# Kernel tuning notes

Hardware: AMD Instinct MI355X
Metric: run time of the kernel (lower is better)

Reference implementation:

```python
import jax, jax.numpy as jnp
import numpy as np

N, E, DIN, DH, ED, H, C = 50000, 800000, 384, 256, 32, 4, 64
EPS = 1e-5


def setup_inputs() -> dict:
    key = jax.random.key(0)
    ks = jax.random.split(key, 32)
    w = lambda k, shape, fan: (jax.random.normal(k, shape, jnp.float32) / np.float32(np.sqrt(fan)))
    inp = {
        'x': jax.random.normal(ks[0], (N, DIN), jnp.float32),
        'edge_index': jax.random.randint(ks[1], (2, E), 0, N, dtype=jnp.int32),
        'edge_attr': jax.random.normal(ks[2], (E, ED), jnp.float32),
        'W_in': w(ks[3], (DIN, DH), DIN), 'b_in': jnp.zeros((DH,), jnp.float32),
        'W_out': w(ks[4], (DH, DH), DH), 'b_out': jnp.zeros((DH,), jnp.float32),
    }
    for i in range(2):
        o = 5 + 6 * i
        inp[f'Wl{i}'] = w(ks[o + 0], (DH, H * C), DH)
        inp[f'bl{i}'] = jnp.zeros((H * C,), jnp.float32)
        inp[f'Wr{i}'] = w(ks[o + 1], (DH, H * C), DH)
        inp[f'br{i}'] = jnp.zeros((H * C,), jnp.float32)
        inp[f'We{i}'] = w(ks[o + 2], (ED, H * C), ED)
        inp[f'att{i}'] = w(ks[o + 3], (H, C), C)
        inp[f'bias{i}'] = jnp.zeros((H * C,), jnp.float32)
        inp[f'g{i}'] = jnp.ones((DH,), jnp.float32)
        inp[f'beta{i}'] = jnp.zeros((DH,), jnp.float32)
    return inp


def _gatv2(h, src, dst, ea, Wl, bl, Wr, br, We, att, bias):
    # h: [N, DH]; src/dst: [Etot]; ea: [Etot, ED]
    xl = (h @ Wl + bl).reshape(N, H, C)
    xr = (h @ Wr + br).reshape(N, H, C)
    ee = (ea @ We).reshape(-1, H, C)
    m = jax.nn.leaky_relu(xl[src] + xr[dst] + ee, 0.2)  # [Etot,H,C]
    logits = jnp.einsum('ehc,hc->eh', m, att)           # [Etot,H]
    mx = jax.ops.segment_max(logits, dst, num_segments=N)
    p = jnp.exp(logits - mx[dst])
    den = jax.ops.segment_sum(p, dst, num_segments=N)
    alpha = p / den[dst]                                # softmax per dst node
    out = jax.ops.segment_sum(xl[src] * alpha[:, :, None], dst, num_segments=N)
    return out.reshape(N, H * C) + bias


def _graph_norm(h, g, beta):
    # PyG LayerNorm(mode='graph'), batch=None: normalize over all nodes & channels
    mu = h.mean()
    hc = h - mu
    var = (hc * hc).mean()
    return hc / jnp.sqrt(var + EPS) * g + beta


def reference(x, edge_index, edge_attr, W_in, b_in,
              Wl0, bl0, Wr0, br0, We0, att0, bias0, g0, beta0,
              Wl1, bl1, Wr1, br1, We1, att1, bias1, g1, beta1,
              W_out, b_out):
    loops = jnp.arange(N, dtype=edge_index.dtype)
    src = jnp.concatenate([edge_index[0], loops])
    dst = jnp.concatenate([edge_index[1], loops])
    # self-loop edge_attr filled with mean edge feature (PyG fill_value='mean')
    ea = jnp.concatenate([edge_attr, jnp.broadcast_to(edge_attr.mean(0), (N, ED))], axis=0)
    h = jax.nn.relu(x @ W_in + b_in)
    layers = ((Wl0, bl0, Wr0, br0, We0, att0, bias0, g0, beta0),
              (Wl1, bl1, Wr1, br1, We1, att1, bias1, g1, beta1))
    for Wl, bl, Wr, br, We, att, bias, g, beta in layers:
        hn = jax.nn.elu(_gatv2(h, src, dst, ea, Wl, bl, Wr, br, We, att, bias))
        h = _graph_norm(h + hn, g, beta)
    return h @ W_out + b_out
```

## Files before the change

### kernel.cpp

```cpp
#include <hip/hip_runtime.h>
#include <hip/hip_bf16.h>

#define N_NODES 50000
#define E_EDGES 800000
#define DIN_K   384
#define DH_N    256
#define EPSN    1e-5f

typedef unsigned short ushortT;
typedef __attribute__((ext_vector_type(4))) float f32x4;
typedef __attribute__((ext_vector_type(8))) short bf16x8;

static __device__ __forceinline__ float bf2f(unsigned short u)
{
    return __uint_as_float(((unsigned)u) << 16);
}
static __device__ __forceinline__ unsigned short f2bf(float f)
{
    unsigned u = __float_as_uint(f);
    unsigned r = (u + 0x7fffu + ((u >> 16) & 1u)) >> 16;
    return (unsigned short)r;
}
static __device__ __forceinline__ unsigned pack2(float a, float b)
{
    return (unsigned)f2bf(a) | ((unsigned)f2bf(b) << 16);
}

__global__ __launch_bounds__(256) void ea_accum_kernel(const float* __restrict__ ea,
                                                       float* __restrict__ accum, long total)
{
    long stride = (long)gridDim.x * blockDim.x;
    float local = 0.f;
    for (long i = (long)blockIdx.x * blockDim.x + threadIdx.x; i < total; i += stride)
        local += ea[i];
    __shared__ float red[256];
    red[threadIdx.x] = local;
    __syncthreads();
    if (threadIdx.x < 32) {
        float s = 0.f;
#pragma unroll
        for (int r = 0; r < 8; ++r) s += red[r * 32 + threadIdx.x];
        atomicAdd(&accum[threadIdx.x], s);
    }
}

__global__ void hist_kernel(const int* __restrict__ dst, int* __restrict__ counts, int E)
{
    int stride = gridDim.x * blockDim.x;
    for (int e = blockIdx.x * blockDim.x + threadIdx.x; e < E; e += stride)
        atomicAdd(&counts[dst[e]], 1);
}

__global__ __launch_bounds__(1024) void scan_kernel(const int* __restrict__ counts,
                                                    int* __restrict__ offsets, int Nn)
{
    __shared__ int sdata[1024];
    __shared__ int run_s;
    int tid = threadIdx.x;
    if (tid == 0) run_s = 0;
    __syncthreads();
    for (int base2 = 0; base2 < Nn; base2 += 1024) {
        int i = base2 + tid;
        int v = (i < Nn) ? counts[i] : 0;
        sdata[tid] = v;
        __syncthreads();
        for (int off = 1; off < 1024; off <<= 1) {
            int t = (tid >= off) ? sdata[tid - off] : 0;
            __syncthreads();
            sdata[tid] += t;
            __syncthreads();
        }
        int run = run_s;
        if (i < Nn) offsets[i] = run + sdata[tid] - v;
        int tot = sdata[1023];
        __syncthreads();
        if (tid == 0) run_s = run + tot;
        __syncthreads();
    }
    if (tid == 0) offsets[Nn] = run_s;
}

__global__ void scatter_kernel(const int* __restrict__ src, const int* __restrict__ dst,
                               const int* __restrict__ offsets, int* __restrict__ cursors,
                               int* __restrict__ s_src, int* __restrict__ s_dst,
                               int* __restrict__ s_eid, int E)
{
    int stride = gridDim.x * blockDim.x;
    for (int e = blockIdx.x * blockDim.x + threadIdx.x; e < E; e += stride) {
        int d = dst[e];
        int p = offsets[d] + atomicAdd(&cursors[d], 1);
        s_src[p] = src[e];
        s_dst[p] = d;
        s_eid[p] = e;
    }
}

__global__ void eemean_kernel(const float* __restrict__ accum,
                              const float* __restrict__ We0, const float* __restrict__ We1,
                              float* __restrict__ eemean, float invE)
{
    int tid = threadIdx.x;
    int layer = tid >> 8, c = tid & 255;
    const float* W = layer ? We1 : We0;
    float s = 0.f;
#pragma unroll
    for (int j = 0; j < 32; ++j) s += accum[j] * invE * W[j * 256 + c];
    eemean[layer * 256 + c] = s;
}

__global__ __launch_bounds__(256) void transpose_bf16_kernel(const float* __restrict__ in,
                                                             ushortT* __restrict__ out,
                                                             int K, int N)
{
    __shared__ float tile[32][33];
    int bx = blockIdx.x * 32;
    int by = blockIdx.y * 32;
    int tx = threadIdx.x & 31, ty = threadIdx.x >> 5;
#pragma unroll
    for (int r = 0; r < 32; r += 8) {
        int k = by + ty + r, n = bx + tx;
        if (k < K && n < N) tile[ty + r][tx] = in[(size_t)k * N + n];
    }
    __syncthreads();
#pragma unroll
    for (int r = 0; r < 32; r += 8) {
        int n = bx + ty + r, k = by + tx;
        if (n < N && k < K) out[(size_t)n * K + k] = f2bf(tile[tx][ty + r]);
    }
}

__global__ void fuse_bias_kernel(const float* __restrict__ bl, const float* __restrict__ br,
                                 float* __restrict__ out)
{
    int i = threadIdx.x;
    out[i] = (i < 256) ? bl[i] : br[i - 256];
}

__global__ __launch_bounds__(256) void mfma_gemm_kernel(
    const float* __restrict__ A, const ushortT* __restrict__ Bt,
    const float* __restrict__ bias, float* __restrict__ Cf,
    ushortT* __restrict__ Cb, int K, int Nn, int act)
{
    __shared__ __align__(16) ushortT As[128 * 32];
    __shared__ __align__(16) ushortT Bs[128 * 32];
    int tid = threadIdx.x;
    int brow = blockIdx.x * 128;
    int bcol = blockIdx.y * 128;
    int lane = tid & 63, w = tid >> 6;
    int wr = w >> 1, wc = w & 1;
    int fr = lane & 15, fq = lane >> 4;

    f32x4 acc[4][4];
#pragma unroll
    for (int i = 0; i < 4; ++i)
#pragma unroll
        for (int j = 0; j < 4; ++j)
            acc[i][j] = (f32x4){0.f, 0.f, 0.f, 0.f};

    int r0 = tid >> 2, g0 = tid & 3;
    int r1 = r0 + 64;
    int arow0 = brow + r0, arow1 = brow + r1;
    bool av0 = arow0 < N_NODES, av1 = arow1 < N_NODES;
    const float* Ap0 = A + (size_t)arow0 * K + g0 * 8;
    const float* Ap1 = A + (size_t)arow1 * K + g0 * 8;
    const ushortT* Bp0 = Bt + (size_t)(bcol + r0) * K + g0 * 8;
    const ushortT* Bp1 = Bt + (size_t)(bcol + r1) * K + g0 * 8;
    uint4* asw0 = (uint4*)&As[(size_t)tid * 8];
    uint4* asw1 = (uint4*)&As[(size_t)(tid + 256) * 8];
    uint4* bsw0 = (uint4*)&Bs[(size_t)tid * 8];
    uint4* bsw1 = (uint4*)&Bs[(size_t)(tid + 256) * 8];

    for (int k0 = 0; k0 < K; k0 += 32) {
        float4 z = make_float4(0.f, 0.f, 0.f, 0.f);
        float4 fa0 = z, fa1 = z, fc0 = z, fc1 = z;
        if (av0) { fa0 = *(const float4*)(Ap0 + k0); fc0 = *(const float4*)(Ap0 + k0 + 4); }
        if (av1) { fa1 = *(const float4*)(Ap1 + k0); fc1 = *(const float4*)(Ap1 + k0 + 4); }
        uint4 ub0 = *(const uint4*)(Bp0 + k0);
        uint4 ub1 = *(const uint4*)(Bp1 + k0);
        uint4 ua0, ua1;
        ua0.x = pack2(fa0.x, fa0.y); ua0.y = pack2(fa0.z, fa0.w);
        ua0.z = pack2(fc0.x, fc0.y); ua0.w = pack2(fc0.z, fc0.w);
        ua1.x = pack2(fa1.x, fa1.y); ua1.y = pack2(fa1.z, fa1.w);
        ua1.z = pack2(fc1.x, fc1.y); ua1.w = pack2(fc1.z, fc1.w);
        __syncthreads();
        *asw0 = ua0; *asw1 = ua1;
        *bsw0 = ub0; *bsw1 = ub1;
        __syncthreads();

        bf16x8 af[4], bfv[4];
#pragma unroll
        for (int mi = 0; mi < 4; ++mi)
            af[mi] = *(bf16x8*)&As[(size_t)(wr * 64 + mi * 16 + fr) * 32 + fq * 8];
#pragma unroll
        for (int ni = 0; ni < 4; ++ni)
            bfv[ni] = *(bf16x8*)&Bs[(size_t)(wc * 64 + ni * 16 + fr) * 32 + fq * 8];
#pragma unroll
        for (int mi = 0; mi < 4; ++mi)
#pragma unroll
            for (int ni = 0; ni < 4; ++ni)
                acc[mi][ni] = __builtin_amdgcn_mfma_f32_16x16x32_bf16(
                    af[mi], bfv[ni], acc[mi][ni], 0, 0, 0);
    }

#pragma unroll
    for (int ni = 0; ni < 4; ++ni) {
        int col = bcol + wc * 64 + ni * 16 + fr;
        float bv = bias[col];
#pragma unroll
        for (int mi = 0; mi < 4; ++mi) {
#pragma unroll
            for (int r = 0; r < 4; ++r) {
                int row = brow + wr * 64 + mi * 16 + fq * 4 + r;
                if (row < N_NODES) {
                    float t = acc[mi][ni][r] + bv;
                    if (act == 1) t = t > 0.f ? t : 0.f;
                    if (Cf) Cf[(size_t)row * Nn + col] = t;
                    if (Cb) Cb[(size_t)row * Nn + col] = f2bf(t);
                }
            }
        }
    }
}

__global__ __launch_bounds__(256) void edge_logits_kernel(
    const float* __restrict__ ea, const int* __restrict__ s_eid,
    const int* __restrict__ s_src, const int* __restrict__ s_dst,
    const ushortT* __restrict__ Wet, const float* __restrict__ att,
    const ushortT* __restrict__ xlr, float* __restrict__ logits)
{
    __shared__ __align__(16) ushortT Wet_lds[256 * 40];
    __shared__ float att_lds[256];
    __shared__ int sidx[64], didx[64], eidv[64];
    int tid = threadIdx.x;
    int brow = blockIdx.x * 64;

#pragma unroll
    for (int t = 0; t < 4; ++t) {
        int f = tid + t * 256;
        int row = f >> 2, q = f & 3;
        *(uint4*)&Wet_lds[row * 40 + q * 8] = *(const uint4*)(Wet + (size_t)row * 32 + q * 8);
    }
    att_lds[tid] = att[tid];
    if (tid < 64) {
        sidx[tid] = s_src[brow + tid];
        didx[tid] = s_dst[brow + tid];
        eidv[tid] = s_eid[brow + tid];
    }
    __syncthreads();

    int lane = tid & 63, w = tid >> 6;
    int fr = lane & 15, fq = lane >> 4;
    int e_lane = w * 16 + fr;

    int eid = eidv[e_lane];
    const float* earow = ea + (size_t)eid * 32 + fq * 8;
    float4 f0 = ((const float4*)earow)[0];
    float4 f1 = ((const float4*)earow)[1];
    union { unsigned u[4]; bf16x8 v; } ub;
    ub.u[0] = pack2(f0.x, f0.y);
    ub.u[1] = pack2(f0.z, f0.w);
    ub.u[2] = pack2(f1.x, f1.y);
    ub.u[3] = pack2(f1.z, f1.w);
    bf16x8 bfrag = ub.v;

    f32x4 acc[16];
#pragma unroll
    for (int mi = 0; mi < 16; ++mi) {
        bf16x8 afrag = *(bf16x8*)&Wet_lds[(mi * 16 + fr) * 40 + fq * 8];
        acc[mi] = __builtin_amdgcn_mfma_f32_16x16x32_bf16(
            afrag, bfrag, (f32x4){0.f, 0.f, 0.f, 0.f}, 0, 0, 0);
    }

    int sn = sidx[e_lane], dn = didx[e_lane];
    const ushortT* lxp = xlr + (size_t)sn * 512;
    const ushortT* rxp = xlr + (size_t)dn * 512 + 256;
    float part[4] = {0.f, 0.f, 0.f, 0.f};
#pragma unroll
    for (int mi = 0; mi < 16; ++mi) {
        int ch = mi * 16 + fq * 4;
        ushort4 lx = *(const ushort4*)(lxp + ch);
        ushort4 rx = *(const ushort4*)(rxp + ch);
        float4 at = *(const float4*)&att_lds[ch];
        float t0 = acc[mi][0] + bf2f(lx.x) + bf2f(rx.x); t0 = t0 > 0.f ? t0 : 0.2f * t0;
        float t1 = acc[mi][1] + bf2f(lx.y) + bf2f(rx.y); t1 = t1 > 0.f ? t1 : 0.2f * t1;
        float t2 = acc[mi][2] + bf2f(lx.z) + bf2f(rx.z); t2 = t2 > 0.f ? t2 : 0.2f * t2;
        float t3 = acc[mi][3] + bf2f(lx.w) + bf2f(rx.w); t3 = t3 > 0.f ? t3 : 0.2f * t3;
        part[mi >> 2] += t0 * at.x + t1 * at.y + t2 * at.z + t3 * at.w;
    }
#pragma unroll
    for (int hh = 0; hh < 4; ++hh) {
        part[hh] += __shfl_xor(part[hh], 16);
        part[hh] += __shfl_xor(part[hh], 32);
    }
    if (fq == 0) {
        float4 o = make_float4(part[0], part[1], part[2], part[3]);
        *(float4*)&logits[(size_t)(brow + e_lane) * 4] = o;
    }
}

__global__ __launch_bounds__(256) void edge_attn_kernel(
    const int* __restrict__ s_src, const int* __restrict__ offsets,
    const float* __restrict__ logits,
    const float* __restrict__ att, const float* __restrict__ bias,
    const float* __restrict__ eemean,
    const ushortT* __restrict__ xlr, float* __restrict__ h)
{
    int lane = threadIdx.x & 63;
    int d = blockIdx.x * 4 + (threadIdx.x >> 6);
    size_t xbase = (size_t)d * 512 + lane * 4;
    size_t hbase = (size_t)d * 256 + lane * 4;
    int head = lane >> 4;

    ushort4 xlu = *(const ushort4*)(xlr + xbase);
    ushort4 xru = *(const ushort4*)(xlr + xbase + 256);
    float xr0 = bf2f(xru.x), xr1 = bf2f(xru.y), xr2 = bf2f(xru.z), xr3 = bf2f(xru.w);
    float xs0 = bf2f(xlu.x), xs1 = bf2f(xlu.y), xs2 = bf2f(xlu.z), xs3 = bf2f(xlu.w);
    float4 eem = *(const float4*)(eemean + lane * 4);
    float4 at4 = *(const float4*)(att + lane * 4);

    float m = -1e30f, s = 0.f;
    float acc0 = 0.f, acc1 = 0.f, acc2 = 0.f, acc3 = 0.f;
    int beg = offsets[d], end = offsets[d + 1];

    int idx1 = 0;
    ushort4 x_cur = make_ushort4(0, 0, 0, 0);
    float lg_cur = 0.f;
    if (beg < end) {
        int idx0 = s_src[beg];
        x_cur = *(const ushort4*)(xlr + (size_t)idx0 * 512 + lane * 4);
        lg_cur = logits[(size_t)beg * 4 + head];
        if (beg + 1 < end) idx1 = s_src[beg + 1];
    }

    for (int pos = beg; pos < end; ++pos) {
        ushort4 xv = x_cur;
        float lg = lg_cur;
        int np = pos + 1;
        if (np < end) {
            x_cur = *(const ushort4*)(xlr + (size_t)idx1 * 512 + lane * 4);
            lg_cur = logits[(size_t)np * 4 + head];
        }
        if (pos + 2 < end) idx1 = s_src[pos + 2];

        float nm = fmaxf(m, lg);
        float sc = __expf(m - nm);
        float pr = __expf(lg - nm);
        float v0 = bf2f(xv.x), v1 = bf2f(xv.y), v2 = bf2f(xv.z), v3 = bf2f(xv.w);
        s = s * sc + pr;
        acc0 = acc0 * sc + pr * v0;
        acc1 = acc1 * sc + pr * v1;
        acc2 = acc2 * sc + pr * v2;
        acc3 = acc3 * sc + pr * v3;
        m = nm;
    }

    {
        float t0 = xs0 + xr0 + eem.x; t0 = t0 > 0.f ? t0 : 0.2f * t0;
        float t1 = xs1 + xr1 + eem.y; t1 = t1 > 0.f ? t1 : 0.2f * t1;
        float t2 = xs2 + xr2 + eem.z; t2 = t2 > 0.f ? t2 : 0.2f * t2;
        float t3 = xs3 + xr3 + eem.w; t3 = t3 > 0.f ? t3 : 0.2f * t3;
        float lg = t0 * at4.x + t1 * at4.y + t2 * at4.z + t3 * at4.w;
        lg += __shfl_xor(lg, 1);
        lg += __shfl_xor(lg, 2);
        lg += __shfl_xor(lg, 4);
        lg += __shfl_xor(lg, 8);
        float nm = fmaxf(m, lg);
        float sc = __expf(m - nm);
        float pr = __expf(lg - nm);
        s = s * sc + pr;
        acc0 = acc0 * sc + pr * xs0;
        acc1 = acc1 * sc + pr * xs1;
        acc2 = acc2 * sc + pr * xs2;
        acc3 = acc3 * sc + pr * xs3;
    }

    float inv = 1.f / s;
    float4 b4 = *(const float4*)(bias + lane * 4);
    float4 hv = *(const float4*)(h + hbase);
    float o0 = acc0 * inv + b4.x; o0 = o0 > 0.f ? o0 : __expf(o0) - 1.f;
    float o1 = acc1 * inv + b4.y; o1 = o1 > 0.f ? o1 : __expf(o1) - 1.f;
    float o2 = acc2 * inv + b4.z; o2 = o2 > 0.f ? o2 : __expf(o2) - 1.f;
    float o3 = acc3 * inv + b4.w; o3 = o3 > 0.f ? o3 : __expf(o3) - 1.f;
    *(float4*)(h + hbase) = make_float4(hv.x + o0, hv.y + o1, hv.z + o2, hv.w + o3);
}

__global__ __launch_bounds__(256) void stats_kernel(const float* __restrict__ h,
                                                    float* __restrict__ stats)
{
    int stride = gridDim.x * blockDim.x;
    int total = N_NODES * 64;
    float ls = 0.f, lq = 0.f;
    for (int i = blockIdx.x * blockDim.x + threadIdx.x; i < total; i += stride) {
        float4 v = ((const float4*)h)[i];
        ls += v.x + v.y + v.z + v.w;
        lq += v.x * v.x + v.y * v.y + v.z * v.z + v.w * v.w;
    }
#pragma unroll
    for (int o = 1; o < 64; o <<= 1) {
        ls += __shfl_xor(ls, o);
        lq += __shfl_xor(lq, o);
    }
    __shared__ float red[8];
    int lane = threadIdx.x & 63, w = threadIdx.x >> 6;
    if (lane == 0) { red[w * 2] = ls; red[w * 2 + 1] = lq; }
    __syncthreads();
    if (threadIdx.x == 0) {
        atomicAdd(&stats[0], red[0] + red[2] + red[4] + red[6]);
        atomicAdd(&stats[1], red[1] + red[3] + red[5] + red[7]);
    }
}

__global__ void norm_finalize_kernel(float* __restrict__ stats)
{
    float invM = 1.f / ((float)N_NODES * 256.f);
    float mu = stats[0] * invM;
    float var = stats[1] * invM - mu * mu;
    stats[2] = mu;
    stats[3] = rsqrtf(var + EPSN);
}

__global__ void normalize_kernel(float* __restrict__ h, const float* __restrict__ g,
                                 const float* __restrict__ beta, const float* __restrict__ stats)
{
    float mu = stats[2], sc = stats[3];
    int stride = gridDim.x * blockDim.x;
    int total = N_NODES * 64;
    for (int i = blockIdx.x * blockDim.x + threadIdx.x; i < total; i += stride) {
        float4 v = ((float4*)h)[i];
        int k = (i & 63) * 4;
        float4 gv = *(const float4*)&g[k];
        float4 bv = *(const float4*)&beta[k];
        v.x = (v.x - mu) * sc * gv.x + bv.x;
        v.y = (v.y - mu) * sc * gv.y + bv.y;
        v.z = (v.z - mu) * sc * gv.z + bv.z;
        v.w = (v.w - mu) * sc * gv.w + bv.w;
        ((float4*)h)[i] = v;
    }
}

extern "C" void kernel_launch(void* const* d_in, const int* in_sizes, int n_in,
                              void* d_out, int out_size, void* d_ws, size_t ws_size,
                              hipStream_t stream)
{
    (void)in_sizes; (void)n_in; (void)out_size; (void)ws_size;
    const float* x     = (const float*)d_in[0];
    const int*   eidx  = (const int*)d_in[1];
    const float* ea    = (const float*)d_in[2];
    const float* W_in  = (const float*)d_in[3];
    const float* b_in  = (const float*)d_in[4];
    const float* W_out = (const float*)d_in[5];
    const float* b_out = (const float*)d_in[6];
    const float* Wl[2]  = {(const float*)d_in[7],  (const float*)d_in[16]};
    const float* bl[2]  = {(const float*)d_in[8],  (const float*)d_in[17]};
    const float* Wr[2]  = {(const float*)d_in[9],  (const float*)d_in[18]};
    const float* br[2]  = {(const float*)d_in[10], (const float*)d_in[19]};
    const float* We[2]  = {(const float*)d_in[11], (const float*)d_in[20]};
    const float* att[2] = {(const float*)d_in[12], (const float*)d_in[21]};
    const float* bias[2]= {(const float*)d_in[13], (const float*)d_in[22]};
    const float* g[2]   = {(const float*)d_in[14], (const float*)d_in[23]};
    const float* beta[2]= {(const float*)d_in[15], (const float*)d_in[24]};

    char* p = (char*)d_ws;
    auto take = [&](size_t bytes) -> char* {
        char* r = p;
        p += (bytes + 255) & ~(size_t)255;
        return r;
    };
    int*   counts  = (int*)take((size_t)N_NODES * 4);
    int*   cursors = (int*)take((size_t)N_NODES * 4);
    float* ea_acc  = (float*)take(32 * 4);
    float* stats   = (float*)take(8 * 4);
    size_t zero_bytes = (size_t)(p - (char*)d_ws);
    int*   offsets = (int*)take((size_t)(N_NODES + 1) * 4);
    int*   s_src   = (int*)take((size_t)E_EDGES * 4);
    int*   s_dst   = (int*)take((size_t)E_EDGES * 4);
    int*   s_eid   = (int*)take((size_t)E_EDGES * 4);
    float* eemean  = (float*)take(512 * 4);
    ushortT* WtIn  = (ushortT*)take((size_t)256 * 384 * 2);
    ushortT* WtLR0 = (ushortT*)take((size_t)512 * 256 * 2);
    ushortT* WtLR1 = (ushortT*)take((size_t)512 * 256 * 2);
    ushortT* WtOut = (ushortT*)take((size_t)256 * 256 * 2);
    ushortT* Wet0  = (ushortT*)take((size_t)256 * 32 * 2);
    ushortT* Wet1  = (ushortT*)take((size_t)256 * 32 * 2);
    float* fb0     = (float*)take(512 * 4);
    float* fb1     = (float*)take(512 * 4);
    ushortT* xlr   = (ushortT*)take((size_t)N_NODES * 512 * 2);
    float* h       = (float*)take((size_t)N_NODES * 256 * 4);
    float* logits  = (float*)take((size_t)E_EDGES * 4 * 4);

    const ushortT* WtLR[2] = {WtLR0, WtLR1};
    const ushortT* Wet[2] = {Wet0, Wet1};
    const float* fb[2] = {fb0, fb1};

    const int* srcv = eidx;
    const int* dstv = eidx + E_EDGES;

    hipMemsetAsync(d_ws, 0, zero_bytes, stream);

    ea_accum_kernel<<<512, 256, 0, stream>>>(ea, ea_acc, (long)E_EDGES * 32);
    hist_kernel<<<1024, 256, 0, stream>>>(dstv, counts, E_EDGES);
    scan_kernel<<<1, 1024, 0, stream>>>(counts, offsets, N_NODES);
    scatter_kernel<<<1024, 256, 0, stream>>>(srcv, dstv, offsets, cursors,
                                             s_src, s_dst, s_eid, E_EDGES);
    eemean_kernel<<<1, 512, 0, stream>>>(ea_acc, We[0], We[1], eemean, 1.0f / (float)E_EDGES);

    transpose_bf16_kernel<<<dim3(8, 12), 256, 0, stream>>>(W_in, WtIn, 384, 256);
    transpose_bf16_kernel<<<dim3(8, 8), 256, 0, stream>>>(Wl[0], WtLR0, 256, 256);
    transpose_bf16_kernel<<<dim3(8, 8), 256, 0, stream>>>(Wr[0], WtLR0 + 256 * 256, 256, 256);
    transpose_bf16_kernel<<<dim3(8, 8), 256, 0, stream>>>(Wl[1], WtLR1, 256, 256);
    transpose_bf16_kernel<<<dim3(8, 8), 256, 0, stream>>>(Wr[1], WtLR1 + 256 * 256, 256, 256);
    transpose_bf16_kernel<<<dim3(8, 8), 256, 0, stream>>>(W_out, WtOut, 256, 256);
    transpose_bf16_kernel<<<dim3(8, 1), 256, 0, stream>>>(We[0], Wet0, 32, 256);
    transpose_bf16_kernel<<<dim3(8, 1), 256, 0, stream>>>(We[1], Wet1, 32, 256);
    fuse_bias_kernel<<<1, 512, 0, stream>>>(bl[0], br[0], fb0);
    fuse_bias_kernel<<<1, 512, 0, stream>>>(bl[1], br[1], fb1);

    mfma_gemm_kernel<<<dim3(391, 2), 256, 0, stream>>>(x, WtIn, b_in, h, nullptr, 384, 256, 1);

    for (int l = 0; l < 2; ++l) {
        mfma_gemm_kernel<<<dim3(391, 4), 256, 0, stream>>>(h, WtLR[l], fb[l], nullptr, xlr,
                                                           256, 512, 0);
        edge_logits_kernel<<<E_EDGES / 64, 256, 0, stream>>>(ea, s_eid, s_src, s_dst,
                                                             Wet[l], att[l], xlr, logits);
        edge_attn_kernel<<<N_NODES / 4, 256, 0, stream>>>(s_src, offsets, logits,
                                                          att[l], bias[l], eemean + l * 256,
                                                          xlr, h);
        stats_kernel<<<2048, 256, 0, stream>>>(h, stats + l * 4);
        norm_finalize_kernel<<<1, 1, 0, stream>>>(stats + l * 4);
        normalize_kernel<<<2048, 256, 0, stream>>>(h, g[l], beta[l], stats + l * 4);
    }
    mfma_gemm_kernel<<<dim3(391, 2), 256, 0, stream>>>(h, WtOut, b_out, (float*)d_out, nullptr,
                                                       256, 256, 0);
}
```

Baseline: 1.373 ms.

## Split edge attention into alpha and accumulate passes, fuse graph-norm stats

Reorders the edge-logit MFMA output rows so each lane owns one head's 64 contiguous channels, which allows 16-byte gathers and drops the cross-lane shuffle reduction. The online-softmax edge_attn kernel is split in two. A new alpha kernel computes per-destination softmax normalisers across 16 parallel edge slots and writes normalised alphas in place. An accum kernel then does a plain weighted gather-sum and also produces the graph-norm statistics, which removes the separate stats pass over h. The cost is an extra pass that reads and writes the logits array, plus a small self-alpha buffer.

```diff
diff --git a/kernel.cpp b/kernel.cpp
--- a/kernel.cpp
+++ b/kernel.cpp
@@ -24,6 +24,13 @@
 static __device__ __forceinline__ unsigned pack2(float a, float b)
 {
     return (unsigned)f2bf(a) | ((unsigned)f2bf(b) << 16);
+}
+static __device__ __forceinline__ void unpack8(uint4 u, float* f)
+{
+    f[0] = bf2f((ushortT)(u.x & 0xffff)); f[1] = bf2f((ushortT)(u.x >> 16));
+    f[2] = bf2f((ushortT)(u.y & 0xffff)); f[3] = bf2f((ushortT)(u.y >> 16));
+    f[4] = bf2f((ushortT)(u.z & 0xffff)); f[5] = bf2f((ushortT)(u.z >> 16));
+    f[6] = bf2f((ushortT)(u.w & 0xffff)); f[7] = bf2f((ushortT)(u.w >> 16));
 }
 
 __global__ __launch_bounds__(256) void ea_accum_kernel(const float* __restrict__ ea,
@@ -237,8 +244,10 @@
 #pragma unroll
     for (int t = 0; t < 4; ++t) {
         int f = tid + t * 256;
-        int row = f >> 2, q = f & 3;
-        *(uint4*)&Wet_lds[row * 40 + q * 8] = *(const uint4*)(Wet + (size_t)row * 32 + q * 8);
+        int sr = f >> 2, q = f & 3;
+        int mi = sr >> 4, j = sr & 15;
+        int ch = ((j >> 2) << 6) + mi * 4 + (j & 3);
+        *(uint4*)&Wet_lds[sr * 40 + q * 8] = *(const uint4*)(Wet + (size_t)ch * 32 + q * 8);
     }
     att_lds[tid] = att[tid];
     if (tid < 64) {
@@ -272,137 +281,155 @@
     }
 
     int sn = sidx[e_lane], dn = didx[e_lane];
-    const ushortT* lxp = xlr + (size_t)sn * 512;
-    const ushortT* rxp = xlr + (size_t)dn * 512 + 256;
-    float part[4] = {0.f, 0.f, 0.f, 0.f};
-#pragma unroll
-    for (int mi = 0; mi < 16; ++mi) {
-        int ch = mi * 16 + fq * 4;
-        ushort4 lx = *(const ushort4*)(lxp + ch);
-        ushort4 rx = *(const ushort4*)(rxp + ch);
-        float4 at = *(const float4*)&att_lds[ch];
-        float t0 = acc[mi][0] + bf2f(lx.x) + bf2f(rx.x); t0 = t0 > 0.f ? t0 : 0.2f * t0;
-        float t1 = acc[mi][1] + bf2f(lx.y) + bf2f(rx.y); t1 = t1 > 0.f ? t1 : 0.2f * t1;
-        float t2 = acc[mi][2] + bf2f(lx.z) + bf2f(rx.z); t2 = t2 > 0.f ? t2 : 0.2f * t2;
-        float t3 = acc[mi][3] + bf2f(lx.w) + bf2f(rx.w); t3 = t3 > 0.f ? t3 : 0.2f * t3;
-        part[mi >> 2] += t0 * at.x + t1 * at.y + t2 * at.z + t3 * at.w;
-    }
-#pragma unroll
-    for (int hh = 0; hh < 4; ++hh) {
-        part[hh] += __shfl_xor(part[hh], 16);
-        part[hh] += __shfl_xor(part[hh], 32);
-    }
-    if (fq == 0) {
-        float4 o = make_float4(part[0], part[1], part[2], part[3]);
-        *(float4*)&logits[(size_t)(brow + e_lane) * 4] = o;
-    }
-}
-
-__global__ __launch_bounds__(256) void edge_attn_kernel(
-    const int* __restrict__ s_src, const int* __restrict__ offsets,
-    const float* __restrict__ logits,
-    const float* __restrict__ att, const float* __restrict__ bias,
-    const float* __restrict__ eemean,
-    const ushortT* __restrict__ xlr, float* __restrict__ h)
+    const ushortT* lxp = xlr + (size_t)sn * 512 + fq * 64;
+    const ushortT* rxp = xlr + (size_t)dn * 512 + 256 + fq * 64;
+    const float* atp = &att_lds[fq * 64];
+    float lgsum = 0.f;
+#pragma unroll
+    for (int m2 = 0; m2 < 8; ++m2) {
+        uint4 lu = *(const uint4*)(lxp + m2 * 8);
+        uint4 ru = *(const uint4*)(rxp + m2 * 8);
+        float lf[8], rf[8];
+        unpack8(lu, lf);
+        unpack8(ru, rf);
+        float4 a0 = *(const float4*)(atp + m2 * 8);
+        float4 a1 = *(const float4*)(atp + m2 * 8 + 4);
+        f32x4 e0 = acc[2 * m2];
+        f32x4 e1 = acc[2 * m2 + 1];
+        float t0 = e0[0] + lf[0] + rf[0]; t0 = t0 > 0.f ? t0 : 0.2f * t0;
+        float t1 = e0[1] + lf[1] + rf[1]; t1 = t1 > 0.f ? t1 : 0.2f * t1;
+        float t2 = e0[2] + lf[2] + rf[2]; t2 = t2 > 0.f ? t2 : 0.2f * t2;
+        float t3 = e0[3] + lf[3] + rf[3]; t3 = t3 > 0.f ? t3 : 0.2f * t3;
+        float t4 = e1[0] + lf[4] + rf[4]; t4 = t4 > 0.f ? t4 : 0.2f * t4;
+        float t5 = e1[1] + lf[5] + rf[5]; t5 = t5 > 0.f ? t5 : 0.2f * t5;
+        float t6 = e1[2] + lf[6] + rf[6]; t6 = t6 > 0.f ? t6 : 0.2f * t6;
+        float t7 = e1[3] + lf[7] + rf[7]; t7 = t7 > 0.f ? t7 : 0.2f * t7;
+        lgsum += t0 * a0.x + t1 * a0.y + t2 * a0.z + t3 * a0.w
+               + t4 * a1.x + t5 * a1.y + t6 * a1.z + t7 * a1.w;
+    }
+    logits[(size_t)(brow + e_lane) * 4 + fq] = lgsum;
+}
+
+__global__ __launch_bounds__(256) void alpha_kernel(
+    const int* __restrict__ offsets, float* __restrict__ logits,
+    const float* __restrict__ att, const float* __restrict__ eemean,
+    const ushortT* __restrict__ xlr, float* __restrict__ self_alpha)
 {
     int lane = threadIdx.x & 63;
     int d = blockIdx.x * 4 + (threadIdx.x >> 6);
     size_t xbase = (size_t)d * 512 + lane * 4;
+
+    ushort4 xlu = *(const ushort4*)(xlr + xbase);
+    ushort4 xru = *(const ushort4*)(xlr + xbase + 256);
+    float4 eem = *(const float4*)(eemean + lane * 4);
+    float4 at4 = *(const float4*)(att + lane * 4);
+    float t0 = bf2f(xlu.x) + bf2f(xru.x) + eem.x; t0 = t0 > 0.f ? t0 : 0.2f * t0;
+    float t1 = bf2f(xlu.y) + bf2f(xru.y) + eem.y; t1 = t1 > 0.f ? t1 : 0.2f * t1;
+    float t2 = bf2f(xlu.z) + bf2f(xru.z) + eem.z; t2 = t2 > 0.f ? t2 : 0.2f * t2;
+    float t3 = bf2f(xlu.w) + bf2f(xru.w) + eem.w; t3 = t3 > 0.f ? t3 : 0.2f * t3;
+    float lgs = t0 * at4.x + t1 * at4.y + t2 * at4.z + t3 * at4.w;
+    lgs += __shfl_xor(lgs, 1);
+    lgs += __shfl_xor(lgs, 2);
+    lgs += __shfl_xor(lgs, 4);
+    lgs += __shfl_xor(lgs, 8);
+    float lgs_me = __shfl(lgs, (lane & 3) << 4);
+
+    int beg = offsets[d], end = offsets[d + 1];
+    int slot = lane >> 2, hd = lane & 3;
+
+    float m = -1e30f, s = 0.f;
+    for (int i = beg + slot; i < end; i += 16) {
+        float lg = logits[(size_t)i * 4 + hd];
+        float nm = fmaxf(m, lg);
+        s = s * __expf(m - nm) + __expf(lg - nm);
+        m = nm;
+    }
+#pragma unroll
+    for (int o = 4; o < 64; o <<= 1) {
+        float m2 = __shfl_xor(m, o);
+        float s2 = __shfl_xor(s, o);
+        float nm = fmaxf(m, m2);
+        s = s * __expf(m - nm) + s2 * __expf(m2 - nm);
+        m = nm;
+    }
+    {
+        float nm = fmaxf(m, lgs_me);
+        s = s * __expf(m - nm) + __expf(lgs_me - nm);
+        m = nm;
+    }
+    float inv = 1.f / s;
+    if (lane < 4) self_alpha[(size_t)d * 4 + lane] = __expf(lgs_me - m) * inv;
+
+    for (int i = beg + slot; i < end; i += 16) {
+        size_t ix = (size_t)i * 4 + hd;
+        logits[ix] = __expf(logits[ix] - m) * inv;
+    }
+}
+
+__global__ __launch_bounds__(256) void accum_kernel(
+    const int* __restrict__ s_src, const int* __restrict__ offsets,
+    const float* __restrict__ alpha, const float* __restrict__ self_alpha,
+    const float* __restrict__ bias, const ushortT* __restrict__ xlr,
+    float* __restrict__ h, float* __restrict__ stats)
+{
+    int lane = threadIdx.x & 63;
+    int wv = threadIdx.x >> 6;
+    int d = blockIdx.x * 4 + wv;
+    size_t xbase = (size_t)d * 512 + lane * 4;
     size_t hbase = (size_t)d * 256 + lane * 4;
     int head = lane >> 4;
 
     ushort4 xlu = *(const ushort4*)(xlr + xbase);
-    ushort4 xru = *(const ushort4*)(xlr + xbase + 256);
-    float xr0 = bf2f(xru.x), xr1 = bf2f(xru.y), xr2 = bf2f(xru.z), xr3 = bf2f(xru.w);
-    float xs0 = bf2f(xlu.x), xs1 = bf2f(xlu.y), xs2 = bf2f(xlu.z), xs3 = bf2f(xlu.w);
-    float4 eem = *(const float4*)(eemean + lane * 4);
-    float4 at4 = *(const float4*)(att + lane * 4);
-
-    float m = -1e30f, s = 0.f;
-    float acc0 = 0.f, acc1 = 0.f, acc2 = 0.f, acc3 = 0.f;
+    float sa = self_alpha[(size_t)d * 4 + head];
+    float acc0 = sa * bf2f(xlu.x);
+    float acc1 = sa * bf2f(xlu.y);
+    float acc2 = sa * bf2f(xlu.z);
+    float acc3 = sa * bf2f(xlu.w);
+
     int beg = offsets[d], end = offsets[d + 1];
 
     int idx1 = 0;
     ushort4 x_cur = make_ushort4(0, 0, 0, 0);
-    float lg_cur = 0.f;
+    float a_cur = 0.f;
     if (beg < end) {
         int idx0 = s_src[beg];
         x_cur = *(const ushort4*)(xlr + (size_t)idx0 * 512 + lane * 4);
-        lg_cur = logits[(size_t)beg * 4 + head];
+        a_cur = alpha[(size_t)beg * 4 + head];
         if (beg + 1 < end) idx1 = s_src[beg + 1];
     }
-
     for (int pos = beg; pos < end; ++pos) {
         ushort4 xv = x_cur;
-        float lg = lg_cur;
+        float av = a_cur;
         int np = pos + 1;
         if (np < end) {
             x_cur = *(const ushort4*)(xlr + (size_t)idx1 * 512 + lane * 4);
-            lg_cur = logits[(size_t)np * 4 + head];
+            a_cur = alpha[(size_t)np * 4 + head];
         }
         if (pos + 2 < end) idx1 = s_src[pos + 2];
-
-        float nm = fmaxf(m, lg);
-        float sc = __expf(m - nm);
-        float pr = __expf(lg - nm);
-        float v0 = bf2f(xv.x), v1 = bf2f(xv.y), v2 = bf2f(xv.z), v3 = bf2f(xv.w);
-        s = s * sc + pr;
-        acc0 = acc0 * sc + pr * v0;
-        acc1 = acc1 * sc + pr * v1;
-        acc2 = acc2 * sc + pr * v2;
-        acc3 = acc3 * sc + pr * v3;
-        m = nm;
-    }
-
-    {
-        float t0 = xs0 + xr0 + eem.x; t0 = t0 > 0.f ? t0 : 0.2f * t0;
-        float t1 = xs1 + xr1 + eem.y; t1 = t1 > 0.f ? t1 : 0.2f * t1;
-        float t2 = xs2 + xr2 + eem.z; t2 = t2 > 0.f ? t2 : 0.2f * t2;
-        float t3 = xs3 + xr3 + eem.w; t3 = t3 > 0.f ? t3 : 0.2f * t3;
-        float lg = t0 * at4.x + t1 * at4.y + t2 * at4.z + t3 * at4.w;
-        lg += __shfl_xor(lg, 1);
-        lg += __shfl_xor(lg, 2);
-        lg += __shfl_xor(lg, 4);
-        lg += __shfl_xor(lg, 8);
-        float nm = fmaxf(m, lg);
-        float sc = __expf(m - nm);
-        float pr = __expf(lg - nm);
-        s = s * sc + pr;
-        acc0 = acc0 * sc + pr * xs0;
-        acc1 = acc1 * sc + pr * xs1;
-        acc2 = acc2 * sc + pr * xs2;
-        acc3 = acc3 * sc + pr * xs3;
-    }
-
-    float inv = 1.f / s;
-    float4 b4 = *(const float4*)(bias + lane * 4);
+        acc0 += av * bf2f(xv.x);
+        acc1 += av * bf2f(xv.y);
+        acc2 += av * bf2f(xv.z);
+        acc3 += av * bf2f(xv.w);
+    }
+
+    float4 b4 = *(const float4*)&bias[lane * 4];
     float4 hv = *(const float4*)(h + hbase);
-    float o0 = acc0 * inv + b4.x; o0 = o0 > 0.f ? o0 : __expf(o0) - 1.f;
-    float o1 = acc1 * inv + b4.y; o1 = o1 > 0.f ? o1 : __expf(o1) - 1.f;
-    float o2 = acc2 * inv + b4.z; o2 = o2 > 0.f ? o2 : __expf(o2) - 1.f;
-    float o3 = acc3 * inv + b4.w; o3 = o3 > 0.f ? o3 : __expf(o3) - 1.f;
-    *(float4*)(h + hbase) = make_float4(hv.x + o0, hv.y + o1, hv.z + o2, hv.w + o3);
-}
-
-__global__ __launch_bounds__(256) void stats_kernel(const float* __restrict__ h,
-                                                    float* __restrict__ stats)
-{
-    int stride = gridDim.x * blockDim.x;
-    int total = N_NODES * 64;
-    float ls = 0.f, lq = 0.f;
-    for (int i = blockIdx.x * blockDim.x + threadIdx.x; i < total; i += stride) {
-        float4 v = ((const float4*)h)[i];
-        ls += v.x + v.y + v.z + v.w;
-        lq += v.x * v.x + v.y * v.y + v.z * v.z + v.w * v.w;
-    }
+    float o0 = acc0 + b4.x; o0 = o0 > 0.f ? o0 : __expf(o0) - 1.f;
+    float o1 = acc1 + b4.y; o1 = o1 > 0.f ? o1 : __expf(o1) - 1.f;
+    float o2 = acc2 + b4.z; o2 = o2 > 0.f ? o2 : __expf(o2) - 1.f;
+    float o3 = acc3 + b4.w; o3 = o3 > 0.f ? o3 : __expf(o3) - 1.f;
+    float y0 = hv.x + o0, y1 = hv.y + o1, y2 = hv.z + o2, y3 = hv.w + o3;
+    *(float4*)(h + hbase) = make_float4(y0, y1, y2, y3);
+
+    float ls = y0 + y1 + y2 + y3;
+    float lq = y0 * y0 + y1 * y1 + y2 * y2 + y3 * y3;
 #pragma unroll
     for (int o = 1; o < 64; o <<= 1) {
         ls += __shfl_xor(ls, o);
         lq += __shfl_xor(lq, o);
     }
     __shared__ float red[8];
-    int lane = threadIdx.x & 63, w = threadIdx.x >> 6;
-    if (lane == 0) { red[w * 2] = ls; red[w * 2 + 1] = lq; }
+    if (lane == 0) { red[wv * 2] = ls; red[wv * 2 + 1] = lq; }
     __syncthreads();
     if (threadIdx.x == 0) {
         atomicAdd(&stats[0], red[0] + red[2] + red[4] + red[6]);
@@ -487,6 +514,7 @@
     ushortT* xlr   = (ushortT*)take((size_t)N_NODES * 512 * 2);
     float* h       = (float*)take((size_t)N_NODES * 256 * 4);
     float* logits  = (float*)take((size_t)E_EDGES * 4 * 4);
+    float* selfa   = (float*)take((size_t)N_NODES * 4 * 4);
 
     const ushortT* WtLR[2] = {WtLR0, WtLR1};
     const ushortT* Wet[2] = {Wet0, Wet1};
@@ -522,10 +550,10 @@
                                                            256, 512, 0);
         edge_logits_kernel<<<E_EDGES / 64, 256, 0, stream>>>(ea, s_eid, s_src, s_dst,
                                                              Wet[l], att[l], xlr, logits);
-        edge_attn_kernel<<<N_NODES / 4, 256, 0, stream>>>(s_src, offsets, logits,
-                                                          att[l], bias[l], eemean + l * 256,
-                                                          xlr, h);
-        stats_kernel<<<2048, 256, 0, stream>>>(h, stats + l * 4);
+        alpha_kernel<<<N_NODES / 4, 256, 0, stream>>>(offsets, logits, att[l],
+                                                      eemean + l * 256, xlr, selfa);
+        accum_kernel<<<N_NODES / 4, 256, 0, stream>>>(s_src, offsets, logits, selfa,
+                                                      bias[l], xlr, h, stats + l * 4);
         norm_finalize_kernel<<<1, 1, 0, stream>>>(stats + l * 4);
         normalize_kernel<<<2048, 256, 0, stream>>>(h, g[l], beta[l], stats + l * 4);
     }
```

After: 1.722 ms. +25.4%, slower.
